# Kernel optimization log

Measured on AMD Instinct MI355X. Metric: run time of the kernel, lower is better.

The kernel has to match this reference:

```python
import jax, jax.numpy as jnp
import numpy as np

B, N, T, C, H = 4, 1024, 12, 256, 8
DK = C // H
SCALE = 1.0 / np.sqrt(DK)


def setup_inputs() -> dict:
    key = jax.random.key(0)
    ks = jax.random.split(key, 16)
    names = ["flow_q", "flow_k", "flow_v", "speed_q", "speed_k", "speed_v"]
    inp = {n: jax.random.normal(ks[i], (B, N, T, C), dtype=jnp.float32) for i, n in enumerate(names)}
    w_scale = 1.0 / np.sqrt(C)  # ~kaiming-uniform-ish magnitude for Linear(C, C)
    wnames = ["w_fq", "w_fk", "w_fv", "w_sq", "w_sk", "w_sv", "w_out"]
    for j, n in enumerate(wnames):
        inp[n] = jax.random.normal(ks[6 + j], (C, C), dtype=jnp.float32) * w_scale
    inp["b_out"] = jnp.zeros((C,), dtype=jnp.float32)
    xav = np.sqrt(2.0 / (T + 1))  # xavier_normal for (T,1) params
    inp["kj"] = jax.random.normal(ks[13], (T, 1), dtype=jnp.float32) * xav
    inp["vf_fs"] = jax.random.normal(ks[14], (T, 1), dtype=jnp.float32) * xav
    return inp


def _heads(x, w):
    # x: [B,N,T,C], w: [C,C] (torch Linear: y = x @ w.T) -> [B,H,N,T,DK]
    y = jnp.einsum('bntc,oc->bnto', x, w)
    return y.reshape(B, N, T, H, DK).transpose(0, 3, 1, 2, 4)


def reference(flow_q, flow_k, flow_v, speed_q, speed_k, speed_v,
              w_fq, w_fk, w_fv, w_sq, w_sk, w_sv, w_out, b_out, kj, vf_fs):
    Qf = _heads(flow_q, w_fq)
    Kf = _heads(flow_k, w_fk)
    Vf = _heads(flow_v, w_fv)
    Qs = _heads(speed_q, w_sq)
    Ks = _heads(speed_k, w_sk)
    Vs = _heads(speed_v, w_sv)

    # FlowSpeed physics transform: Kj * (v - v^2 / (Vf + 1e-5)); (T,1) broadcasts over (T, DK)
    qf_from_speed = kj * (Qs - jnp.square(Qs) / (vf_fs + 1e-5))

    def att(a, b):  # scores over temporal axis: [B,H,N,T,T] -> softmax
        return jax.nn.softmax(jnp.einsum('bhntd,bhnsd->bhnts', a, b) * SCALE, axis=-1)

    def ctx(z, v):
        return jnp.einsum('bhnts,bhnsd->bhntd', z, v)

    z_ff = att(Qf, Kf)
    z_fs = att(Kf, qf_from_speed)
    z_sf = att(Ks, Qf)
    z_ss = att(Qs, Ks)

    def out_proj(c):  # [B,H,N,T,DK] -> [B,N,T,C] -> fc_out (shared weights)
        c = c.transpose(0, 2, 3, 1, 4).reshape(B, N, T, C)
        return jnp.einsum('bntc,oc->bnto', c, w_out) + b_out

    return (out_proj(ctx(z_ff, Vf)),
            out_proj(ctx(z_fs, Vf)),
            out_proj(ctx(z_sf, Vs)),
            out_proj(ctx(z_ss, Vs)))
```

## Files before the change

kernel.cpp:

```cpp
#include <hip/hip_runtime.h>

#define Bn 4
#define Nn 1024
#define Tn 12
#define Cn 256
#define Hn 8
#define DKn 32
#define Mrows 49152
#define NEl 12582912LL
#define SCALE_ 0.17677669529663687f

typedef __attribute__((ext_vector_type(4))) float f32x4;
typedef __attribute__((ext_vector_type(8))) short s16x8;
typedef __attribute__((ext_vector_type(4))) short s16x4;

__device__ __forceinline__ ushort f2bfu(float x) {
    unsigned u = __builtin_bit_cast(unsigned, x);
    u += 0x7fffu + ((u >> 16) & 1u);
    return (ushort)(u >> 16);
}
__device__ __forceinline__ float bfu2f(ushort h) {
    return __builtin_bit_cast(float, ((unsigned)h) << 16);
}

__device__ __forceinline__ void gld_lds16(const void* g, void* l) {
    __builtin_amdgcn_global_load_lds(
        (const __attribute__((address_space(1))) unsigned*)g,
        (__attribute__((address_space(3))) unsigned*)l, 16, 0, 0);
}

struct WPtrs { const float* src[7]; };

__global__ __launch_bounds__(256)
void wconv_k(WPtrs w, ushort* __restrict__ Wh, ushort* __restrict__ Wl) {
    int idx = blockIdx.x * 256 + threadIdx.x;
    int which = idx >> 16, pos = idx & 65535;
    float x = w.src[which][pos];
    ushort h = f2bfu(x);
    Wh[idx] = h;
    Wl[idx] = f2bfu(x - bfu2f(h));
}

struct GPtrs {
    const void*   A[4];
    const ushort* Wh[4];
    const ushort* Wl[4];
    void*         Y[4];
};

template<bool SPLIT, bool IN_BF16, bool OUT_BF16, bool BIAS>
__device__ __forceinline__ void gemm_body(GPtrs p, const float* __restrict__ bias) {
    const int bt   = blockIdx.y;
    const int bm   = blockIdx.x * 128;
    const int tid  = threadIdx.x;
    const int lane = tid & 63;
    const int wave = tid >> 6;
    const int wm   = wave >> 2;
    const int wn   = wave & 3;
    const int r16  = lane & 15;
    const int cbf  = (lane >> 4) * 16;

    constexpr int ASZ = 128 * 32;
    constexpr int BSZ = 256 * 32;
    __shared__ ushort Ah[2][ASZ];
    __shared__ ushort Bh[2][BSZ];
    __shared__ ushort Al[SPLIT ? 2 : 1][SPLIT ? ASZ : 8];
    __shared__ ushort Bl[SPLIT ? 2 : 1][SPLIT ? BSZ : 8];

    f32x4 acc[4][4];
#pragma unroll
    for (int i = 0; i < 4; i++)
#pragma unroll
        for (int j = 0; j < 4; j++)
            acc[i][j] = (f32x4){0.f, 0.f, 0.f, 0.f};

    auto stage = [&](int buf, int k0) {
#pragma unroll
        for (int c = 0; c < 2; ++c) {
            int ob = c * 8192 + wave * 1024 + lane * 16;
            int r  = ob >> 6;
            int cg = ((ob >> 4) & 3) ^ ((r >> 1) & 3);
            size_t goff = (size_t)r * 256 + k0 + cg * 8;
            void* ldst = (char*)&Bh[buf][0] + c * 8192 + wave * 1024;
            gld_lds16(p.Wh[bt] + goff, ldst);
            if constexpr (SPLIT) {
                void* ldstl = (char*)&Bl[buf][0] + c * 8192 + wave * 1024;
                gld_lds16(p.Wl[bt] + goff, ldstl);
            }
        }
        if constexpr (IN_BF16) {
            int ob = wave * 1024 + lane * 16;
            int r  = ob >> 6;
            int cg = ((ob >> 4) & 3) ^ ((r >> 1) & 3);
            const ushort* g = (const ushort*)p.A[bt] + (size_t)(bm + r) * 256 + k0 + cg * 8;
            void* ldst = (char*)&Ah[buf][0] + wave * 1024;
            gld_lds16(g, ldst);
        } else {
            int r  = tid >> 2;
            int cg = (tid & 3) ^ ((r >> 1) & 3);
            const float* g = (const float*)p.A[bt] + (size_t)(bm + r) * 256 + k0 + cg * 8;
            f32x4 v0 = *(const f32x4*)g;
            f32x4 v1 = *(const f32x4*)(g + 4);
            s16x8 hi, lo;
#pragma unroll
            for (int j = 0; j < 8; j++) {
                float x = (j < 4) ? v0[j] : v1[j - 4];
                ushort hb = f2bfu(x);
                hi[j] = (short)hb;
                if constexpr (SPLIT) lo[j] = (short)f2bfu(x - bfu2f(hb));
            }
            *(s16x8*)((char*)&Ah[buf][0] + tid * 16) = hi;
            if constexpr (SPLIT) *(s16x8*)((char*)&Al[buf][0] + tid * 16) = lo;
        }
    };

    auto compute = [&](int buf) {
        s16x8 a[4], al[4];
#pragma unroll
        for (int mi = 0; mi < 4; mi++) {
            int R   = wm * 64 + mi * 16 + r16;
            int off = (R * 64 + cbf) ^ (((R >> 1) & 3) << 4);
            a[mi] = *(const s16x8*)((const char*)&Ah[buf][0] + off);
            if constexpr (SPLIT) al[mi] = *(const s16x8*)((const char*)&Al[buf][0] + off);
        }
#pragma unroll
        for (int ni = 0; ni < 4; ni++) {
            int R   = wn * 64 + ni * 16 + r16;
            int off = (R * 64 + cbf) ^ (((R >> 1) & 3) << 4);
            s16x8 b = *(const s16x8*)((const char*)&Bh[buf][0] + off);
            s16x8 bl;
            if constexpr (SPLIT) bl = *(const s16x8*)((const char*)&Bl[buf][0] + off);
#pragma unroll
            for (int mi = 0; mi < 4; mi++) {
                acc[mi][ni] = __builtin_amdgcn_mfma_f32_16x16x32_bf16(a[mi], b, acc[mi][ni], 0, 0, 0);
                if constexpr (SPLIT) {
                    acc[mi][ni] = __builtin_amdgcn_mfma_f32_16x16x32_bf16(al[mi], b,  acc[mi][ni], 0, 0, 0);
                    acc[mi][ni] = __builtin_amdgcn_mfma_f32_16x16x32_bf16(a[mi],  bl, acc[mi][ni], 0, 0, 0);
                }
            }
        }
    };

    stage(0, 0);
    __syncthreads();
#pragma unroll
    for (int ks = 0; ks < 8; ++ks) {
        if (ks < 7) stage((ks + 1) & 1, (ks + 1) * 32);
        compute(ks & 1);
        __syncthreads();
    }

#pragma unroll
    for (int mi = 0; mi < 4; mi++) {
#pragma unroll
        for (int ni = 0; ni < 4; ni++) {
            int col  = wn * 64 + ni * 16 + r16;
            int row0 = bm + wm * 64 + mi * 16 + (lane >> 4) * 4;
            float bv = BIAS ? bias[col] : 0.f;
#pragma unroll
            for (int rg = 0; rg < 4; rg++) {
                float v = acc[mi][ni][rg] + bv;
                size_t idx = (size_t)(row0 + rg) * 256 + col;
                if constexpr (OUT_BF16) ((ushort*)p.Y[bt])[idx] = f2bfu(v);
                else                    ((float*)p.Y[bt])[idx]  = v;
            }
        }
    }
}

__global__ __launch_bounds__(512, 4)
void gemm_proj_k(GPtrs p) { gemm_body<false, false, true, false>(p, nullptr); }

__global__ __launch_bounds__(512, 2)
void gemm_split_k(GPtrs p) { gemm_body<true, false, false, false>(p, nullptr); }

__global__ __launch_bounds__(512, 4)
void gemm_out_k(GPtrs p, const float* __restrict__ bias) {
    gemm_body<false, true, false, true>(p, bias);
}


#define VSTR 268

__device__ __forceinline__ s16x8 zero8() { s16x8 z = {0,0,0,0,0,0,0,0}; return z; }

__device__ __forceinline__ void split8(f32x4 a, f32x4 b, s16x8& hi, s16x8& lo) {
#pragma unroll
    for (int j = 0; j < 8; j++) {
        float x = (j < 4) ? a[j] : b[j - 4];
        ushort h = f2bfu(x);
        hi[j] = (short)h;
        lo[j] = (short)f2bfu(x - bfu2f(h));
    }
}

__device__ __forceinline__ void softmax_swapped(f32x4 acc, int g, s16x8& ph, s16x8& pl) {
    float x0 = acc[0] * SCALE_, x1 = acc[1] * SCALE_;
    float x2 = acc[2] * SCALE_, x3 = acc[3] * SCALE_;
    float m = fmaxf(fmaxf(x0, x1), fmaxf(x2, x3));
    m = fmaxf(m, __shfl_xor(m, 16));
    m = fmaxf(m, __shfl_xor(m, 32));
    float e0 = expf(x0 - m), e1 = expf(x1 - m), e2 = expf(x2 - m), e3 = expf(x3 - m);
    if (g == 3) { e0 = 0.f; e1 = 0.f; e2 = 0.f; e3 = 0.f; }
    float s = e0 + e1 + e2 + e3;
    s += __shfl_xor(s, 16);
    s += __shfl_xor(s, 32);
    float inv = 1.f / s;
    float p0 = e0 * inv, p1 = e1 * inv, p2 = e2 * inv, p3 = e3 * inv;
    float q0 = __shfl_down(p0, 16), q1 = __shfl_down(p1, 16);
    float q2 = __shfl_down(p2, 16), q3 = __shfl_down(p3, 16);
    float w[8];
    if (g == 0) { w[0]=p0; w[1]=p1; w[2]=p2; w[3]=p3; w[4]=q0; w[5]=q1; w[6]=q2; w[7]=q3; }
    else if (g == 1) { w[0]=q0; w[1]=q1; w[2]=q2; w[3]=q3; w[4]=0.f; w[5]=0.f; w[6]=0.f; w[7]=0.f; }
    else { w[0]=0.f; w[1]=0.f; w[2]=0.f; w[3]=0.f; w[4]=0.f; w[5]=0.f; w[6]=0.f; w[7]=0.f; }
#pragma unroll
    for (int j = 0; j < 8; j++) {
        ushort h = f2bfu(w[j]);
        ph[j] = (short)h;
        pl[j] = (short)f2bfu(w[j] - bfu2f(h));
    }
}

__device__ __forceinline__ s16x8 load_vfrag(const ushort* sV, int col, int g) {
    s16x8 v = zero8();
    if (g < 2) {
#pragma unroll
        for (int j = 0; j < 8; j++) {
            int s = 8 * g + j;
            if (s < 12) v[j] = (short)sV[s * VSTR + col];
        }
    }
    return v;
}

__device__ __forceinline__ void ctx_store(s16x8 ph, s16x8 pl, s16x8 vb0, s16x8 vb1,
                                          ushort* __restrict__ dst, size_t abase,
                                          int g, int r16) {
    f32x4 zf = {0.f, 0.f, 0.f, 0.f};
    f32x4 o0 = __builtin_amdgcn_mfma_f32_16x16x32_bf16(ph, vb0, zf, 0, 0, 0);
    o0 = __builtin_amdgcn_mfma_f32_16x16x32_bf16(pl, vb0, o0, 0, 0, 0);
    f32x4 o1 = __builtin_amdgcn_mfma_f32_16x16x32_bf16(ph, vb1, zf, 0, 0, 0);
    o1 = __builtin_amdgcn_mfma_f32_16x16x32_bf16(pl, vb1, o1, 0, 0, 0);
    if (g < 3) {
#pragma unroll
        for (int rg = 0; rg < 4; rg++) {
            size_t row = (size_t)(4 * g + rg) * Cn;
            dst[abase + row + r16]      = f2bfu(o0[rg]);
            dst[abase + row + 16 + r16] = f2bfu(o1[rg]);
        }
    }
}

__global__ __launch_bounds__(512)
void attn_k(const ushort* __restrict__ Qf, const float* __restrict__ Kf,
            const ushort* __restrict__ Vf, const float* __restrict__ Qs,
            const ushort* __restrict__ Ks, const ushort* __restrict__ Vs,
            const float* __restrict__ kj, const float* __restrict__ vf_fs,
            ushort* __restrict__ c0, ushort* __restrict__ c1,
            ushort* __restrict__ c2, ushort* __restrict__ c3)
{
    const int bn   = blockIdx.x;
    const int tid  = threadIdx.x;
    const int wave = tid >> 6;
    const int lane = tid & 63;
    const int g    = lane >> 4;
    const int r16  = lane & 15;

    __shared__ ushort sVf[12 * VSTR];
    __shared__ ushort sVs[12 * VSTR];

    if (tid < 384) {
        int t = tid >> 5;
        int c = (tid & 31) * 8;
        size_t gb = (size_t)bn * (Tn * Cn) + (size_t)t * Cn + c;
        s16x8 vf8 = *(const s16x8*)(Vf + gb);
        s16x8 vs8 = *(const s16x8*)(Vs + gb);
        s16x4 a0 = {vf8[0], vf8[1], vf8[2], vf8[3]};
        s16x4 a1 = {vf8[4], vf8[5], vf8[6], vf8[7]};
        s16x4 b0 = {vs8[0], vs8[1], vs8[2], vs8[3]};
        s16x4 b1 = {vs8[4], vs8[5], vs8[6], vs8[7]};
        *(s16x4*)&sVf[t * VSTR + c]     = a0;
        *(s16x4*)&sVf[t * VSTR + c + 4] = a1;
        *(s16x4*)&sVs[t * VSTR + c]     = b0;
        *(s16x4*)&sVs[t * VSTR + c + 4] = b1;
    }

    const int  t    = r16;
    const bool tv   = t < 12;
    const int  d0   = g * 8;
    const size_t abase = (size_t)bn * (Tn * Cn) + (size_t)wave * DKn;
    const size_t rb    = abase + (size_t)t * Cn + d0;

    f32x4 z4 = {0.f, 0.f, 0.f, 0.f};
    s16x8 fQf = tv ? *(const s16x8*)(Qf + rb) : zero8();
    s16x8 fKs = tv ? *(const s16x8*)(Ks + rb) : zero8();

    f32x4 kfa = tv ? *(const f32x4*)(Kf + rb)     : z4;
    f32x4 kfb = tv ? *(const f32x4*)(Kf + rb + 4) : z4;
    f32x4 qsa = tv ? *(const f32x4*)(Qs + rb)     : z4;
    f32x4 qsb = tv ? *(const f32x4*)(Qs + rb + 4) : z4;

    s16x8 fKfh, fKfl, fQsh, fQsl;
    split8(kfa, kfb, fKfh, fKfl);
    split8(qsa, qsb, fQsh, fQsl);

    float kjt  = tv ? kj[t]    : 0.f;
    float vft  = tv ? vf_fs[t] : 0.f;
    float invv = 1.f / (vft + 1e-5f);
    f32x4 qfa, qfb;
#pragma unroll
    for (int j = 0; j < 4; j++) {
        float qa = qsa[j], qb = qsb[j];
        qfa[j] = kjt * (qa - qa * qa * invv);
        qfb[j] = kjt * (qb - qb * qb * invv);
    }
    s16x8 fqfh, fqfl;
    split8(qfa, qfb, fqfh, fqfl);

    f32x4 zf = {0.f, 0.f, 0.f, 0.f};
    f32x4 aff = __builtin_amdgcn_mfma_f32_16x16x32_bf16(fKfh, fQf, zf, 0, 0, 0);
    aff = __builtin_amdgcn_mfma_f32_16x16x32_bf16(fKfl, fQf, aff, 0, 0, 0);
    f32x4 afs = __builtin_amdgcn_mfma_f32_16x16x32_bf16(fqfh, fKfh, zf, 0, 0, 0);
    afs = __builtin_amdgcn_mfma_f32_16x16x32_bf16(fqfl, fKfh, afs, 0, 0, 0);
    afs = __builtin_amdgcn_mfma_f32_16x16x32_bf16(fqfh, fKfl, afs, 0, 0, 0);
    afs = __builtin_amdgcn_mfma_f32_16x16x32_bf16(fqfl, fKfl, afs, 0, 0, 0);
    f32x4 asf = __builtin_amdgcn_mfma_f32_16x16x32_bf16(fQf, fKs, zf, 0, 0, 0);
    f32x4 ass = __builtin_amdgcn_mfma_f32_16x16x32_bf16(fKs, fQsh, zf, 0, 0, 0);
    ass = __builtin_amdgcn_mfma_f32_16x16x32_bf16(fKs, fQsl, ass, 0, 0, 0);

    __syncthreads();
    s16x8 vbf0 = load_vfrag(sVf, wave * 32 + r16,      g);
    s16x8 vbf1 = load_vfrag(sVf, wave * 32 + 16 + r16, g);
    s16x8 vbs0 = load_vfrag(sVs, wave * 32 + r16,      g);
    s16x8 vbs1 = load_vfrag(sVs, wave * 32 + 16 + r16, g);

    s16x8 ph, pl;
    softmax_swapped(aff, g, ph, pl);
    ctx_store(ph, pl, vbf0, vbf1, c0, abase, g, r16);
    softmax_swapped(afs, g, ph, pl);
    ctx_store(ph, pl, vbf0, vbf1, c1, abase, g, r16);
    softmax_swapped(asf, g, ph, pl);
    ctx_store(ph, pl, vbs0, vbs1, c2, abase, g, r16);
    softmax_swapped(ass, g, ph, pl);
    ctx_store(ph, pl, vbs0, vbs1, c3, abase, g, r16);
}

extern "C" void kernel_launch(void* const* d_in, const int* in_sizes, int n_in,
                              void* d_out, int out_size, void* d_ws, size_t ws_size,
                              hipStream_t stream) {
    (void)in_sizes; (void)n_in; (void)out_size; (void)ws_size;

    const float* flow_q  = (const float*)d_in[0];
    const float* flow_k  = (const float*)d_in[1];
    const float* flow_v  = (const float*)d_in[2];
    const float* speed_q = (const float*)d_in[3];
    const float* speed_k = (const float*)d_in[4];
    const float* speed_v = (const float*)d_in[5];
    const float* w_fq  = (const float*)d_in[6];
    const float* w_fk  = (const float*)d_in[7];
    const float* w_fv  = (const float*)d_in[8];
    const float* w_sq  = (const float*)d_in[9];
    const float* w_sk  = (const float*)d_in[10];
    const float* w_sv  = (const float*)d_in[11];
    const float* w_out = (const float*)d_in[12];
    const float* b_out = (const float*)d_in[13];
    const float* kj    = (const float*)d_in[14];
    const float* vf    = (const float*)d_in[15];

    char* ws = (char*)d_ws;
    size_t off = 0;
    auto alloc = [&](size_t bytes) -> void* {
        void* p = ws + off;
        off += (bytes + 255) & ~(size_t)255;
        return p;
    };
    ushort* Wh = (ushort*)alloc(7 * 65536 * 2);
    ushort* Wl = (ushort*)alloc(7 * 65536 * 2);
    ushort* Qf = (ushort*)alloc(NEl * 2);
    float*  Kf = (float*) alloc(NEl * 4);
    ushort* Vf = (ushort*)alloc(NEl * 2);
    float*  Qs = (float*) alloc(NEl * 4);
    ushort* Ks = (ushort*)alloc(NEl * 2);
    ushort* Vs = (ushort*)alloc(NEl * 2);
    ushort* c0 = (ushort*)alloc(NEl * 2);
    ushort* c1 = (ushort*)alloc(NEl * 2);
    ushort* c2 = (ushort*)alloc(NEl * 2);
    ushort* c3 = (ushort*)alloc(NEl * 2);

    float* out = (float*)d_out;

    WPtrs wp;
    wp.src[0] = w_fq; wp.src[1] = w_fk; wp.src[2] = w_fv; wp.src[3] = w_sq;
    wp.src[4] = w_sk; wp.src[5] = w_sv; wp.src[6] = w_out;
    wconv_k<<<dim3(7 * 65536 / 256), 256, 0, stream>>>(wp, Wh, Wl);

    GPtrs p1;
    p1.A[0] = flow_q;  p1.Wh[0] = Wh + 0 * 65536; p1.Wl[0] = Wl + 0 * 65536; p1.Y[0] = Qf;
    p1.A[1] = flow_v;  p1.Wh[1] = Wh + 2 * 65536; p1.Wl[1] = Wl + 2 * 65536; p1.Y[1] = Vf;
    p1.A[2] = speed_k; p1.Wh[2] = Wh + 4 * 65536; p1.Wl[2] = Wl + 4 * 65536; p1.Y[2] = Ks;
    p1.A[3] = speed_v; p1.Wh[3] = Wh + 5 * 65536; p1.Wl[3] = Wl + 5 * 65536; p1.Y[3] = Vs;
    gemm_proj_k<<<dim3(Mrows / 128, 4), 512, 0, stream>>>(p1);

    GPtrs p2;
    p2.A[0] = flow_k;  p2.Wh[0] = Wh + 1 * 65536; p2.Wl[0] = Wl + 1 * 65536; p2.Y[0] = Kf;
    p2.A[1] = speed_q; p2.Wh[1] = Wh + 3 * 65536; p2.Wl[1] = Wl + 3 * 65536; p2.Y[1] = Qs;
    p2.A[2] = flow_k;  p2.Wh[2] = Wh + 1 * 65536; p2.Wl[2] = Wl + 1 * 65536; p2.Y[2] = Kf;
    p2.A[3] = flow_k;  p2.Wh[3] = Wh + 1 * 65536; p2.Wl[3] = Wl + 1 * 65536; p2.Y[3] = Kf;
    gemm_split_k<<<dim3(Mrows / 128, 2), 512, 0, stream>>>(p2);

    attn_k<<<dim3(Bn * Nn), 512, 0, stream>>>(Qf, Kf, Vf, Qs, Ks, Vs, kj, vf, c0, c1, c2, c3);

    GPtrs p3;
    p3.A[0] = c0; p3.Wh[0] = Wh + 6 * 65536; p3.Wl[0] = Wl + 6 * 65536; p3.Y[0] = out;
    p3.A[1] = c1; p3.Wh[1] = Wh + 6 * 65536; p3.Wl[1] = Wl + 6 * 65536; p3.Y[1] = out + NEl;
    p3.A[2] = c2; p3.Wh[2] = Wh + 6 * 65536; p3.Wl[2] = Wl + 6 * 65536; p3.Y[2] = out + 2 * NEl;
    p3.A[3] = c3; p3.Wh[3] = Wh + 6 * 65536; p3.Wl[3] = Wl + 6 * 65536; p3.Y[3] = out + 3 * NEl;
    gemm_out_k<<<dim3(Mrows / 128, 4), 512, 0, stream>>>(p3, b_out);
}
```

Baseline: 601.9 us.

## Fuse output projection into attention kernel via LDS-staged context

Merges the attention kernel and the output-projection GEMM into one kernel. Each block writes its four 12x256 context tiles into swizzled LDS and multiplies them by w_out, which is streamed through LDS in 32-column slices, then adds the bias and writes fp32 output directly. This removes the four bf16 context buffers and their global write/read round trip, plus one kernel launch. In exchange every block re-reads the full 256x256 w_out, the MFMA tiles are only 12/16 occupied, and the larger LDS footprint may lower occupancy.

```diff
diff --git a/kernel.cpp b/kernel.cpp
--- a/kernel.cpp
+++ b/kernel.cpp
@@ -48,8 +48,8 @@
     void*         Y[4];
 };
 
-template<bool SPLIT, bool IN_BF16, bool OUT_BF16, bool BIAS>
-__device__ __forceinline__ void gemm_body(GPtrs p, const float* __restrict__ bias) {
+template<bool SPLIT, bool IN_BF16, bool OUT_BF16>
+__device__ __forceinline__ void gemm_body(GPtrs p) {
     const int bt   = blockIdx.y;
     const int bm   = blockIdx.x * 128;
     const int tid  = threadIdx.x;
@@ -156,10 +156,9 @@
         for (int ni = 0; ni < 4; ni++) {
             int col  = wn * 64 + ni * 16 + r16;
             int row0 = bm + wm * 64 + mi * 16 + (lane >> 4) * 4;
-            float bv = BIAS ? bias[col] : 0.f;
 #pragma unroll
             for (int rg = 0; rg < 4; rg++) {
-                float v = acc[mi][ni][rg] + bv;
+                float v = acc[mi][ni][rg];
                 size_t idx = (size_t)(row0 + rg) * 256 + col;
                 if constexpr (OUT_BF16) ((ushort*)p.Y[bt])[idx] = f2bfu(v);
                 else                    ((float*)p.Y[bt])[idx]  = v;
@@ -169,18 +168,11 @@
 }
 
 __global__ __launch_bounds__(512, 4)
-void gemm_proj_k(GPtrs p) { gemm_body<false, false, true, false>(p, nullptr); }
+void gemm_proj_k(GPtrs p) { gemm_body<false, false, true>(p); }
 
 __global__ __launch_bounds__(512, 2)
-void gemm_split_k(GPtrs p) { gemm_body<true, false, false, false>(p, nullptr); }
-
-__global__ __launch_bounds__(512, 4)
-void gemm_out_k(GPtrs p, const float* __restrict__ bias) {
-    gemm_body<false, true, false, true>(p, bias);
-}
-
-
-#define VSTR 268
+void gemm_split_k(GPtrs p) { gemm_body<true, false, false>(p); }
+
 
 __device__ __forceinline__ s16x8 zero8() { s16x8 z = {0,0,0,0,0,0,0,0}; return z; }
 
@@ -221,6 +213,8 @@
     }
 }
 
+#define VSTR 268
+
 __device__ __forceinline__ s16x8 load_vfrag(const ushort* sV, int col, int g) {
     s16x8 v = zero8();
     if (g < 2) {
@@ -233,31 +227,34 @@
     return v;
 }
 
-__device__ __forceinline__ void ctx_store(s16x8 ph, s16x8 pl, s16x8 vb0, s16x8 vb1,
-                                          ushort* __restrict__ dst, size_t abase,
-                                          int g, int r16) {
+__device__ __forceinline__ void ctx_to_lds(ushort* smem, s16x8 ph, s16x8 pl,
+                                           s16x8 vb0, s16x8 vb1,
+                                           int mat, int head, int g, int r16) {
     f32x4 zf = {0.f, 0.f, 0.f, 0.f};
     f32x4 o0 = __builtin_amdgcn_mfma_f32_16x16x32_bf16(ph, vb0, zf, 0, 0, 0);
     o0 = __builtin_amdgcn_mfma_f32_16x16x32_bf16(pl, vb0, o0, 0, 0, 0);
     f32x4 o1 = __builtin_amdgcn_mfma_f32_16x16x32_bf16(ph, vb1, zf, 0, 0, 0);
     o1 = __builtin_amdgcn_mfma_f32_16x16x32_bf16(pl, vb1, o1, 0, 0, 0);
     if (g < 3) {
+        int grp = head * 4 + (r16 >> 3);
+        int c7  = r16 & 7;
 #pragma unroll
         for (int rg = 0; rg < 4; rg++) {
-            size_t row = (size_t)(4 * g + rg) * Cn;
-            dst[abase + row + r16]      = f2bfu(o0[rg]);
-            dst[abase + row + 16 + r16] = f2bfu(o1[rg]);
+            int t = 4 * g + rg;
+            int base = 8192 + mat * 3072 + t * 256 + c7;
+            smem[base + (((grp    ) ^ (t & 7)) << 3)] = f2bfu(o0[rg]);
+            smem[base + (((grp + 2) ^ (t & 7)) << 3)] = f2bfu(o1[rg]);
         }
     }
 }
 
 __global__ __launch_bounds__(512)
-void attn_k(const ushort* __restrict__ Qf, const float* __restrict__ Kf,
-            const ushort* __restrict__ Vf, const float* __restrict__ Qs,
-            const ushort* __restrict__ Ks, const ushort* __restrict__ Vs,
-            const float* __restrict__ kj, const float* __restrict__ vf_fs,
-            ushort* __restrict__ c0, ushort* __restrict__ c1,
-            ushort* __restrict__ c2, ushort* __restrict__ c3)
+void attn_out_k(const ushort* __restrict__ Qf, const float* __restrict__ Kf,
+                const ushort* __restrict__ Vf, const float* __restrict__ Qs,
+                const ushort* __restrict__ Ks, const ushort* __restrict__ Vs,
+                const float* __restrict__ kj, const float* __restrict__ vf_fs,
+                const ushort* __restrict__ Wo, const float* __restrict__ b_out,
+                float* __restrict__ out)
 {
     const int bn   = blockIdx.x;
     const int tid  = threadIdx.x;
@@ -266,9 +263,19 @@
     const int g    = lane >> 4;
     const int r16  = lane & 15;
 
-    __shared__ ushort sVf[12 * VSTR];
-    __shared__ ushort sVs[12 * VSTR];
-
+    __shared__ ushort smem[20480];
+
+    const int wo_row  = tid >> 1;
+    const int wo_cg0  = (tid & 1) * 2;
+    const int wo_swz  = (wo_row >> 1) & 3;
+    const int wslot0  = wo_cg0 ^ wo_swz;
+    const int wslot1  = (wo_cg0 + 1) ^ wo_swz;
+    const ushort* wgb = Wo + (size_t)wo_row * 256 + wo_cg0 * 8;
+    s16x8 wa = *(const s16x8*)(wgb);
+    s16x8 wb = *(const s16x8*)(wgb + 8);
+
+    ushort* sVf = smem;
+    ushort* sVs = smem + 12 * VSTR;
     if (tid < 384) {
         int t = tid >> 5;
         int c = (tid & 31) * 8;
@@ -336,13 +343,59 @@
 
     s16x8 ph, pl;
     softmax_swapped(aff, g, ph, pl);
-    ctx_store(ph, pl, vbf0, vbf1, c0, abase, g, r16);
+    ctx_to_lds(smem, ph, pl, vbf0, vbf1, 0, wave, g, r16);
     softmax_swapped(afs, g, ph, pl);
-    ctx_store(ph, pl, vbf0, vbf1, c1, abase, g, r16);
+    ctx_to_lds(smem, ph, pl, vbf0, vbf1, 1, wave, g, r16);
     softmax_swapped(asf, g, ph, pl);
-    ctx_store(ph, pl, vbs0, vbs1, c2, abase, g, r16);
+    ctx_to_lds(smem, ph, pl, vbs0, vbs1, 2, wave, g, r16);
     softmax_swapped(ass, g, ph, pl);
-    ctx_store(ph, pl, vbs0, vbs1, c3, abase, g, r16);
+    ctx_to_lds(smem, ph, pl, vbs0, vbs1, 3, wave, g, r16);
+
+    const int mat  = wave >> 1;
+    const int half = wave & 1;
+
+    f32x4 oacc[8];
+#pragma unroll
+    for (int ni = 0; ni < 8; ni++) oacc[ni] = (f32x4){0.f, 0.f, 0.f, 0.f};
+
+#pragma unroll
+    for (int ks = 0; ks < 8; ks++) {
+        __syncthreads();
+        *(s16x8*)&smem[wo_row * 32 + (wslot0 << 3)] = wa;
+        *(s16x8*)&smem[wo_row * 32 + (wslot1 << 3)] = wb;
+        s16x8 na = wa, nb = wb;
+        if (ks < 7) {
+            const ushort* wg2 = Wo + (size_t)wo_row * 256 + (ks + 1) * 32 + wo_cg0 * 8;
+            na = *(const s16x8*)(wg2);
+            nb = *(const s16x8*)(wg2 + 8);
+        }
+        __syncthreads();
+        s16x8 a = zero8();
+        if (r16 < 12)
+            a = *(const s16x8*)&smem[8192 + mat * 3072 + r16 * 256 +
+                                     (((ks * 4 + g) ^ (r16 & 7)) << 3)];
+#pragma unroll
+        for (int ni = 0; ni < 8; ni++) {
+            int o = half * 128 + ni * 16 + r16;
+            s16x8 b = *(const s16x8*)&smem[o * 32 + ((g ^ ((o >> 1) & 3)) << 3)];
+            oacc[ni] = __builtin_amdgcn_mfma_f32_16x16x32_bf16(a, b, oacc[ni], 0, 0, 0);
+        }
+        wa = na; wb = nb;
+    }
+
+    float* outp = out + (size_t)mat * NEl + (size_t)bn * (Tn * Cn);
+    if (g < 3) {
+#pragma unroll
+        for (int ni = 0; ni < 8; ni++) {
+            int o = half * 128 + ni * 16 + r16;
+            float bv = b_out[o];
+#pragma unroll
+            for (int rg = 0; rg < 4; rg++) {
+                int tt = g * 4 + rg;
+                outp[(size_t)tt * Cn + o] = oacc[ni][rg] + bv;
+            }
+        }
+    }
 }
 
 extern "C" void kernel_launch(void* const* d_in, const int* in_sizes, int n_in,
@@ -382,10 +435,6 @@
     float*  Qs = (float*) alloc(NEl * 4);
     ushort* Ks = (ushort*)alloc(NEl * 2);
     ushort* Vs = (ushort*)alloc(NEl * 2);
-    ushort* c0 = (ushort*)alloc(NEl * 2);
-    ushort* c1 = (ushort*)alloc(NEl * 2);
-    ushort* c2 = (ushort*)alloc(NEl * 2);
-    ushort* c3 = (ushort*)alloc(NEl * 2);
 
     float* out = (float*)d_out;
 
@@ -408,12 +457,6 @@
     p2.A[3] = flow_k;  p2.Wh[3] = Wh + 1 * 65536; p2.Wl[3] = Wl + 1 * 65536; p2.Y[3] = Kf;
     gemm_split_k<<<dim3(Mrows / 128, 2), 512, 0, stream>>>(p2);
 
-    attn_k<<<dim3(Bn * Nn), 512, 0, stream>>>(Qf, Kf, Vf, Qs, Ks, Vs, kj, vf, c0, c1, c2, c3);
-
-    GPtrs p3;
-    p3.A[0] = c0; p3.Wh[0] = Wh + 6 * 65536; p3.Wl[0] = Wl + 6 * 65536; p3.Y[0] = out;
-    p3.A[1] = c1; p3.Wh[1] = Wh + 6 * 65536; p3.Wl[1] = Wl + 6 * 65536; p3.Y[1] = out + NEl;
-    p3.A[2] = c2; p3.Wh[2] = Wh + 6 * 65536; p3.Wl[2] = Wl + 6 * 65536; p3.Y[2] = out + 2 * NEl;
-    p3.A[3] = c3; p3.Wh[3] = Wh + 6 * 65536; p3.Wl[3] = Wl + 6 * 65536; p3.Y[3] = out + 3 * NEl;
-    gemm_out_k<<<dim3(Mrows / 128, 4), 512, 0, stream>>>(p3, b_out);
-}
+    attn_out_k<<<dim3(Bn * Nn), 512, 0, stream>>>(Qf, Kf, Vf, Qs, Ks, Vs, kj, vf,
+                                                  Wh + 6 * 65536, b_out, out);
+}
```

Measured after the change: 594.0 us. Within noise of the previous version (-1.3%).
